# Kernel tuning notes

Hardware: AMD Instinct MI355X
Metric: run time of the kernel (lower is better)

## Reference

```python
import jax, jax.numpy as jnp
import numpy as np

B, C, H, W, D = 2, 96, 64, 64, 32
NUM_HEADS = 8

def setup_inputs() -> dict:
    key = jax.random.key(0)
    kx, kq, kk, kv, kp = jax.random.split(key, 5)
    x = jax.random.normal(kx, (B, C, H, W, D), dtype=jnp.float32)
    # torch nn.Linear weights: [out_features, in_features]; 1x1x1 conv proj as [C_out, C_in]
    s = 0.02
    Wq = jax.random.normal(kq, (C, C), dtype=jnp.float32) * s
    Wk = jax.random.normal(kk, (C, C), dtype=jnp.float32) * s
    Wv = jax.random.normal(kv, (C, C), dtype=jnp.float32) * s
    Wproj = jax.random.normal(kp, (C, C), dtype=jnp.float32) * s
    return {"x": x, "Wq": Wq, "Wk": Wk, "Wv": Wv, "Wproj": Wproj}

def reference(x, Wq, Wk, Wv, Wproj):
    b, c, h, w, d = x.shape
    n = h * w * d
    nh = NUM_HEADS
    hd = c // nh  # head dim (qk_dim == v_dim == dim here)
    # [B, C, H, W, D] -> [B, N, C]
    xf = jnp.transpose(x.reshape(b, c, n), (0, 2, 1))
    def to_heads(W):
        y = jnp.einsum('bnc,oc->bno', xf, W)  # nn.Linear: x @ W^T
        return jnp.transpose(y.reshape(b, n, nh, hd), (0, 2, 1, 3))  # [B, H, N, hd]
    q = to_heads(Wq)
    k = to_heads(Wk)
    v = to_heads(Wv)
    q = jax.nn.softmax(q, axis=-1)   # over head dim
    k = jax.nn.softmax(k, axis=-2)   # over tokens N
    # linear attention: contract over N first -> tiny [B, H, hd, hd] context
    context = jnp.einsum('bhnd,bhne->bhde', k, v)
    attn = jnp.einsum('bhnd,bhde->bhne', q, context)  # [B, H, N, hd]
    out = jnp.transpose(attn, (0, 2, 1, 3)).reshape(b, n, c)  # [B, N, C]
    out = jnp.transpose(out, (0, 2, 1)).reshape(b, c, h, w, d)
    # 1x1x1 conv projection (bias=False) == channel mixing
    out = jnp.einsum('oc,bchwd->bohwd', Wproj, out)
    return out
```

## Files before the change

### kernel.cpp

```cpp
#include <hip/hip_runtime.h>


typedef _Float16 half_t;
typedef _Float16 half8 __attribute__((ext_vector_type(8)));
typedef float f32x4 __attribute__((ext_vector_type(4)));

#define MFMA16 __builtin_amdgcn_mfma_f32_16x16x32_f16
#define NSH 17
#define NP 16

__global__ __launch_bounds__(256, 2)
void p1(const float* __restrict__ x, const float* __restrict__ Wk,
        const float* __restrict__ Wv, float* __restrict__ part) {
  __shared__ __align__(16) char smem[73792];
  half_t* xs  = (half_t*)smem;
  half_t* wsm = (half_t*)(smem + 26624);
  half_t* vl  = (half_t*)smem;
  half_t* ke  = (half_t*)(smem + 46592);

  const int tid  = threadIdx.x;
  const int lane = tid & 63, l15 = lane & 15, quad = lane >> 4, wid = tid >> 6;
  const int b  = blockIdx.x >> 10;
  const int n0 = (blockIdx.x & 1023) << 7;

  {
    const int n = tid & 127, cg = tid >> 7;
    const float* xb = x + (((size_t)(b * 96 + cg * 48)) << NSH) + n0 + n;
#pragma unroll
    for (int i = 0; i < 48; ++i)
      xs[n * 104 + cg * 48 + i] = (half_t)xb[(size_t)i << NSH];
  }
#pragma unroll
  for (int i = 0; i < 36; ++i) {
    int id = i * 256 + tid; int o = id / 96, c = id - o * 96;
    wsm[o * 104 + c] = (half_t)Wk[id];
  }
  __syncthreads();

  f32x4 acc[6][2];
#pragma unroll
  for (int rt = 0; rt < 6; ++rt)
#pragma unroll
    for (int ct = 0; ct < 2; ++ct) acc[rt][ct] = (f32x4){0.f, 0.f, 0.f, 0.f};
#pragma unroll
  for (int ks = 0; ks < 3; ++ks) {
    half8 af[6], bf[2];
#pragma unroll
    for (int rt = 0; rt < 6; ++rt)
      af[rt] = *(const half8*)&wsm[(rt * 16 + l15) * 104 + ks * 32 + quad * 8];
#pragma unroll
    for (int ct = 0; ct < 2; ++ct)
      bf[ct] = *(const half8*)&xs[((wid * 2 + ct) * 16 + l15) * 104 + ks * 32 + quad * 8];
#pragma unroll
    for (int rt = 0; rt < 6; ++rt)
#pragma unroll
      for (int ct = 0; ct < 2; ++ct)
        acc[rt][ct] = MFMA16(af[rt], bf[ct], acc[rt][ct], 0, 0, 0);
  }
#pragma unroll
  for (int rt = 0; rt < 6; ++rt)
#pragma unroll
    for (int ct = 0; ct < 2; ++ct)
#pragma unroll
      for (int i = 0; i < 4; ++i) {
        int row = rt * 16 + quad * 4 + i;
        int col = (wid * 2 + ct) * 16 + l15;
        ke[row * 136 + col] = (half_t)__expf(acc[rt][ct][i]);
      }
  __syncthreads();

#pragma unroll
  for (int i = 0; i < 36; ++i) {
    int id = i * 256 + tid; int o = id / 96, c = id - o * 96;
    wsm[o * 104 + c] = (half_t)Wv[id];
  }
  __syncthreads();

#pragma unroll
  for (int rt = 0; rt < 6; ++rt)
#pragma unroll
    for (int ct = 0; ct < 2; ++ct) acc[rt][ct] = (f32x4){0.f, 0.f, 0.f, 0.f};
#pragma unroll
  for (int ks = 0; ks < 3; ++ks) {
    half8 af[6], bf[2];
#pragma unroll
    for (int rt = 0; rt < 6; ++rt)
      af[rt] = *(const half8*)&wsm[(rt * 16 + l15) * 104 + ks * 32 + quad * 8];
#pragma unroll
    for (int ct = 0; ct < 2; ++ct)
      bf[ct] = *(const half8*)&xs[((wid * 2 + ct) * 16 + l15) * 104 + ks * 32 + quad * 8];
#pragma unroll
    for (int rt = 0; rt < 6; ++rt)
#pragma unroll
      for (int ct = 0; ct < 2; ++ct)
        acc[rt][ct] = MFMA16(af[rt], bf[ct], acc[rt][ct], 0, 0, 0);
  }
  __syncthreads();
#pragma unroll
  for (int rt = 0; rt < 6; ++rt)
#pragma unroll
    for (int ct = 0; ct < 2; ++ct)
#pragma unroll
      for (int i = 0; i < 4; ++i) {
        int row = rt * 16 + quad * 4 + i;
        int col = (wid * 2 + ct) * 16 + l15;
        vl[row * 136 + col] = (half_t)acc[rt][ct][i];
      }
  __syncthreads();

  float* dst = part + (size_t)((blockIdx.x & (NP - 1)) * 2 + b) * 1248;
#pragma unroll
  for (int hh = 0; hh < 2; ++hh) {
    const int h = wid * 2 + hh;
    f32x4 c = (f32x4){0.f, 0.f, 0.f, 0.f};
#pragma unroll
    for (int ks = 0; ks < 4; ++ks) {
      half8 a  = *(const half8*)&ke[(h * 12 + l15) * 136 + ks * 32 + quad * 8];
      half8 bv = *(const half8*)&vl[(h * 12 + l15) * 136 + ks * 32 + quad * 8];
      c = MFMA16(a, bv, c, 0, 0, 0);
    }
#pragma unroll
    for (int i = 0; i < 4; ++i) {
      int d = quad * 4 + i, e = l15;
      if (d < 12 && e < 12) atomicAdd(&dst[h * 144 + d * 12 + e], c[i]);
    }
  }
  if (tid < 96) {
    float s = 0.f;
#pragma unroll
    for (int j = 0; j < 16; ++j) {
      half8 v = *(const half8*)&ke[tid * 136 + j * 8];
#pragma unroll
      for (int e = 0; e < 8; ++e) s += (float)v[e];
    }
    atomicAdd(&dst[1152 + tid], s);
  }
}

__global__ void kB(const float* __restrict__ part, const float* __restrict__ Wproj,
                   float* __restrict__ Mt) {
  const int g = blockIdx.x * 256 + threadIdx.x;
  const int b = g / (96 * 96);
  const int rem = g % (96 * 96);
  const int o = rem / 96;
  const int r = rem % 96;
  const int h = r / 12, d = r % 12;
  float s = 0.f;
#pragma unroll
  for (int p = 0; p < NP; ++p) s += part[(size_t)(p * 2 + b) * 1248 + 1152 + r];
  float acc = 0.f;
#pragma unroll
  for (int e = 0; e < 12; ++e) {
    float ce = 0.f;
#pragma unroll
    for (int p = 0; p < NP; ++p)
      ce += part[(size_t)(p * 2 + b) * 1248 + h * 144 + d * 12 + e];
    acc = fmaf(ce, Wproj[o * 96 + h * 12 + e], acc);
  }
  Mt[(size_t)(b * 96 + o) * 96 + r] = acc / s;
}

__global__ __launch_bounds__(256, 2)
void p3(const float* __restrict__ x, const float* __restrict__ Wq,
        const float* __restrict__ Mt, float* __restrict__ out) {
  __shared__ __align__(16) char smem[66560];
  half_t* xs  = (half_t*)smem;
  half_t* wsm = (half_t*)(smem + 26624);
  half_t* Ms  = (half_t*)(smem + 46592);
  half_t* qs  = (half_t*)smem;

  const int tid  = threadIdx.x;
  const int lane = tid & 63, l15 = lane & 15, quad = lane >> 4, wid = tid >> 6;
  const int b  = blockIdx.x >> 10;
  const int n0 = (blockIdx.x & 1023) << 7;

  {
    const int n = tid & 127, cg = tid >> 7;
    const float* xb = x + (((size_t)(b * 96 + cg * 48)) << NSH) + n0 + n;
#pragma unroll
    for (int i = 0; i < 48; ++i)
      xs[n * 104 + cg * 48 + i] = (half_t)xb[(size_t)i << NSH];
  }
#pragma unroll
  for (int i = 0; i < 36; ++i) {
    int id = i * 256 + tid; int o = id / 96, c = id - o * 96;
    wsm[o * 104 + c] = (half_t)Wq[id];
  }
  {
    const float* mtb = Mt + (size_t)b * 9216;
#pragma unroll
    for (int i = 0; i < 36; ++i) {
      int id = i * 256 + tid; int o = id / 96, r = id - o * 96;
      Ms[o * 104 + r] = (half_t)mtb[id];
    }
  }
  __syncthreads();

  f32x4 acc[6][2];
#pragma unroll
  for (int rt = 0; rt < 6; ++rt)
#pragma unroll
    for (int ct = 0; ct < 2; ++ct) acc[rt][ct] = (f32x4){0.f, 0.f, 0.f, 0.f};
#pragma unroll
  for (int ks = 0; ks < 3; ++ks) {
    half8 af[6], bf[2];
#pragma unroll
    for (int rt = 0; rt < 6; ++rt)
      af[rt] = *(const half8*)&wsm[(rt * 16 + l15) * 104 + ks * 32 + quad * 8];
#pragma unroll
    for (int ct = 0; ct < 2; ++ct)
      bf[ct] = *(const half8*)&xs[((wid * 2 + ct) * 16 + l15) * 104 + ks * 32 + quad * 8];
#pragma unroll
    for (int rt = 0; rt < 6; ++rt)
#pragma unroll
      for (int ct = 0; ct < 2; ++ct)
        acc[rt][ct] = MFMA16(af[rt], bf[ct], acc[rt][ct], 0, 0, 0);
  }
  __syncthreads();
#pragma unroll
  for (int rt = 0; rt < 6; ++rt)
#pragma unroll
    for (int ct = 0; ct < 2; ++ct)
#pragma unroll
      for (int i = 0; i < 4; ++i) {
        int row = rt * 16 + quad * 4 + i;
        int col = (wid * 2 + ct) * 16 + l15;
        qs[col * 104 + row] = (half_t)acc[rt][ct][i];
      }
  __syncthreads();

  {
    const int n = tid & 127, hg = tid >> 7;
    half8 v[6];
#pragma unroll
    for (int j = 0; j < 6; ++j)
      v[j] = *(const half8*)&qs[n * 104 + hg * 48 + j * 8];
    float q[48];
#pragma unroll
    for (int j = 0; j < 6; ++j)
#pragma unroll
      for (int e = 0; e < 8; ++e) q[j * 8 + e] = (float)v[j][e];
#pragma unroll
    for (int hh = 0; hh < 4; ++hh) {
      float* ql = q + hh * 12;
      float m = ql[0];
#pragma unroll
      for (int j = 1; j < 12; ++j) m = fmaxf(m, ql[j]);
      float s = 0.f;
#pragma unroll
      for (int j = 0; j < 12; ++j) { ql[j] = __expf(ql[j] - m); s += ql[j]; }
      const float inv = 1.0f / s;
#pragma unroll
      for (int j = 0; j < 12; ++j) ql[j] *= inv;
    }
#pragma unroll
    for (int j = 0; j < 6; ++j) {
      half8 w;
#pragma unroll
      for (int e = 0; e < 8; ++e) w[e] = (half_t)q[j * 8 + e];
      *(half8*)&qs[n * 104 + hg * 48 + j * 8] = w;
    }
  }
  __syncthreads();

#pragma unroll
  for (int rt = 0; rt < 6; ++rt)
#pragma unroll
    for (int ct = 0; ct < 2; ++ct) acc[rt][ct] = (f32x4){0.f, 0.f, 0.f, 0.f};
#pragma unroll
  for (int ks = 0; ks < 3; ++ks) {
    half8 af[6], bf[2];
#pragma unroll
    for (int rt = 0; rt < 6; ++rt)
      af[rt] = *(const half8*)&Ms[(rt * 16 + l15) * 104 + ks * 32 + quad * 8];
#pragma unroll
    for (int ct = 0; ct < 2; ++ct)
      bf[ct] = *(const half8*)&qs[((wid * 2 + ct) * 16 + l15) * 104 + ks * 32 + quad * 8];
#pragma unroll
    for (int rt = 0; rt < 6; ++rt)
#pragma unroll
      for (int ct = 0; ct < 2; ++ct)
        acc[rt][ct] = MFMA16(af[rt], bf[ct], acc[rt][ct], 0, 0, 0);
  }
#pragma unroll
  for (int rt = 0; rt < 6; ++rt)
#pragma unroll
    for (int ct = 0; ct < 2; ++ct)
#pragma unroll
      for (int i = 0; i < 4; ++i) {
        int row = rt * 16 + quad * 4 + i;
        int col = (wid * 2 + ct) * 16 + l15;
        out[(((size_t)(b * 96 + row)) << NSH) + n0 + col] = acc[rt][ct][i];
      }
}

extern "C" void kernel_launch(void* const* d_in, const int* in_sizes, int n_in,
                              void* d_out, int out_size, void* d_ws, size_t ws_size,
                              hipStream_t stream) {
  const float* x     = (const float*)d_in[0];
  const float* Wq    = (const float*)d_in[1];
  const float* Wk    = (const float*)d_in[2];
  const float* Wv    = (const float*)d_in[3];
  const float* Wproj = (const float*)d_in[4];
  float* out = (float*)d_out;
  float* ws  = (float*)d_ws;

  float* part = ws;
  float* Mt   = ws + NP * 2 * 1248;

  hipMemsetAsync(part, 0, NP * 2 * 1248 * sizeof(float), stream);
  p1<<<2048, 256, 0, stream>>>(x, Wk, Wv, part);
  kB<<<72, 256, 0, stream>>>(part, Wproj, Mt);
  p3<<<2048, 256, 0, stream>>>(x, Wq, Mt, out);
}
```

Baseline: 264.7 us.

## Make p1/p3 persistent over four token tiles with register-resident weights and prefetch

Each block now handles 512 tokens in four 128-token tiles instead of one, so the grid shrinks from 2048 to 512 blocks. Weight fragments (Wk/Wv, Wq, Mt) are converted once into MFMA operand registers rather than staged through shared memory per block. The next tile of x is prefetched into registers while the current tile's MFMAs run, and the context and key-sum partials are accumulated across tiles, which cuts the number of global atomics. p3 now writes its output as vectorized f32x4 stores, and the MFMA operand roles are swapped to match. The trade-off is higher register pressure and fewer blocks to hide latency.

```diff
diff --git a/kernel.cpp b/kernel.cpp
--- a/kernel.cpp
+++ b/kernel.cpp
@@ -2,8 +2,9 @@
 
 
 typedef _Float16 half_t;
-typedef _Float16 half8 __attribute__((ext_vector_type(8)));
-typedef float f32x4 __attribute__((ext_vector_type(4)));
+typedef _Float16 half4v __attribute__((ext_vector_type(4)));
+typedef _Float16 half8  __attribute__((ext_vector_type(8)));
+typedef float    f32x4  __attribute__((ext_vector_type(4)));
 
 #define MFMA16 __builtin_amdgcn_mfma_f32_16x16x32_f16
 #define NSH 17
@@ -12,129 +13,150 @@
 __global__ __launch_bounds__(256, 2)
 void p1(const float* __restrict__ x, const float* __restrict__ Wk,
         const float* __restrict__ Wv, float* __restrict__ part) {
-  __shared__ __align__(16) char smem[73792];
-  half_t* xs  = (half_t*)smem;
-  half_t* wsm = (half_t*)(smem + 26624);
-  half_t* vl  = (half_t*)smem;
-  half_t* ke  = (half_t*)(smem + 46592);
+  __shared__ __align__(16) char smem[79392];
+  half_t* xs = (half_t*)smem;
+  half_t* ke = (half_t*)(smem + 26624);
+  half_t* vl = (half_t*)(smem + 53008);
 
   const int tid  = threadIdx.x;
   const int lane = tid & 63, l15 = lane & 15, quad = lane >> 4, wid = tid >> 6;
-  const int b  = blockIdx.x >> 10;
-  const int n0 = (blockIdx.x & 1023) << 7;
-
+  const int w0 = wid & 1, w1 = wid >> 1;
+  const int b  = blockIdx.x >> 8;
+  const int n0 = (blockIdx.x & 255) << 9;
+  const float* xb = x + (((size_t)b * 96) << NSH);
+
+  half8 wkB[3][3], wvB[3][3];
+#pragma unroll
+  for (int ct = 0; ct < 3; ++ct)
+#pragma unroll
+    for (int ks = 0; ks < 3; ++ks) {
+      const int row = 48 * w1 + ct * 16 + l15;
+      const float* pk = Wk + row * 96 + ks * 32 + quad * 8;
+      const float* pv = Wv + row * 96 + ks * 32 + quad * 8;
+      half8 hk, hv;
+#pragma unroll
+      for (int j = 0; j < 8; ++j) { hk[j] = (half_t)pk[j]; hv[j] = (half_t)pv[j]; }
+      wkB[ct][ks] = hk; wvB[ct][ks] = hv;
+    }
+
+  const int sn = tid & 127, scg = tid >> 7;
   {
-    const int n = tid & 127, cg = tid >> 7;
-    const float* xb = x + (((size_t)(b * 96 + cg * 48)) << NSH) + n0 + n;
+    float xr[48];
 #pragma unroll
     for (int i = 0; i < 48; ++i)
-      xs[n * 104 + cg * 48 + i] = (half_t)xb[(size_t)i << NSH];
-  }
-#pragma unroll
-  for (int i = 0; i < 36; ++i) {
-    int id = i * 256 + tid; int o = id / 96, c = id - o * 96;
-    wsm[o * 104 + c] = (half_t)Wk[id];
-  }
+      xr[i] = xb[(((size_t)(scg * 48 + i)) << NSH) + n0 + sn];
+#pragma unroll
+    for (int j = 0; j < 12; ++j) {
+      half4v h;
+#pragma unroll
+      for (int e = 0; e < 4; ++e) h[e] = (half_t)xr[4 * j + e];
+      *(half4v*)&xs[sn * 104 + scg * 48 + 4 * j] = h;
+    }
+  }
+  f32x4 ctxa[2] = {{0.f,0.f,0.f,0.f},{0.f,0.f,0.f,0.f}};
+  float sacc = 0.f;
   __syncthreads();
 
-  f32x4 acc[6][2];
-#pragma unroll
-  for (int rt = 0; rt < 6; ++rt)
-#pragma unroll
-    for (int ct = 0; ct < 2; ++ct) acc[rt][ct] = (f32x4){0.f, 0.f, 0.f, 0.f};
-#pragma unroll
-  for (int ks = 0; ks < 3; ++ks) {
-    half8 af[6], bf[2];
-#pragma unroll
-    for (int rt = 0; rt < 6; ++rt)
-      af[rt] = *(const half8*)&wsm[(rt * 16 + l15) * 104 + ks * 32 + quad * 8];
-#pragma unroll
-    for (int ct = 0; ct < 2; ++ct)
-      bf[ct] = *(const half8*)&xs[((wid * 2 + ct) * 16 + l15) * 104 + ks * 32 + quad * 8];
-#pragma unroll
-    for (int rt = 0; rt < 6; ++rt)
-#pragma unroll
-      for (int ct = 0; ct < 2; ++ct)
-        acc[rt][ct] = MFMA16(af[rt], bf[ct], acc[rt][ct], 0, 0, 0);
-  }
-#pragma unroll
-  for (int rt = 0; rt < 6; ++rt)
-#pragma unroll
-    for (int ct = 0; ct < 2; ++ct)
-#pragma unroll
-      for (int i = 0; i < 4; ++i) {
-        int row = rt * 16 + quad * 4 + i;
-        int col = (wid * 2 + ct) * 16 + l15;
-        ke[row * 136 + col] = (half_t)__expf(acc[rt][ct][i]);
-      }
-  __syncthreads();
-
-#pragma unroll
-  for (int i = 0; i < 36; ++i) {
-    int id = i * 256 + tid; int o = id / 96, c = id - o * 96;
-    wsm[o * 104 + c] = (half_t)Wv[id];
-  }
-  __syncthreads();
-
-#pragma unroll
-  for (int rt = 0; rt < 6; ++rt)
-#pragma unroll
-    for (int ct = 0; ct < 2; ++ct) acc[rt][ct] = (f32x4){0.f, 0.f, 0.f, 0.f};
-#pragma unroll
-  for (int ks = 0; ks < 3; ++ks) {
-    half8 af[6], bf[2];
-#pragma unroll
-    for (int rt = 0; rt < 6; ++rt)
-      af[rt] = *(const half8*)&wsm[(rt * 16 + l15) * 104 + ks * 32 + quad * 8];
-#pragma unroll
-    for (int ct = 0; ct < 2; ++ct)
-      bf[ct] = *(const half8*)&xs[((wid * 2 + ct) * 16 + l15) * 104 + ks * 32 + quad * 8];
-#pragma unroll
-    for (int rt = 0; rt < 6; ++rt)
-#pragma unroll
-      for (int ct = 0; ct < 2; ++ct)
-        acc[rt][ct] = MFMA16(af[rt], bf[ct], acc[rt][ct], 0, 0, 0);
-  }
-  __syncthreads();
-#pragma unroll
-  for (int rt = 0; rt < 6; ++rt)
-#pragma unroll
-    for (int ct = 0; ct < 2; ++ct)
-#pragma unroll
-      for (int i = 0; i < 4; ++i) {
-        int row = rt * 16 + quad * 4 + i;
-        int col = (wid * 2 + ct) * 16 + l15;
-        vl[row * 136 + col] = (half_t)acc[rt][ct][i];
-      }
-  __syncthreads();
-
+  for (int t = 0; t < 4; ++t) {
+    float xr[48];
+    if (t < 3) {
+#pragma unroll
+      for (int i = 0; i < 48; ++i)
+        xr[i] = xb[(((size_t)(scg * 48 + i)) << NSH) + n0 + (t + 1) * 128 + sn];
+    }
+    f32x4 acc[4][3];
+#pragma unroll
+    for (int rt = 0; rt < 4; ++rt)
+#pragma unroll
+      for (int ct = 0; ct < 3; ++ct) acc[rt][ct] = (f32x4){0.f,0.f,0.f,0.f};
+#pragma unroll
+    for (int ks = 0; ks < 3; ++ks) {
+      half8 af[4];
+#pragma unroll
+      for (int rt = 0; rt < 4; ++rt)
+        af[rt] = *(const half8*)&xs[(64 * w0 + rt * 16 + l15) * 104 + ks * 32 + quad * 8];
+#pragma unroll
+      for (int rt = 0; rt < 4; ++rt)
+#pragma unroll
+        for (int ct = 0; ct < 3; ++ct)
+          acc[rt][ct] = MFMA16(af[rt], wkB[ct][ks], acc[rt][ct], 0, 0, 0);
+    }
+#pragma unroll
+    for (int rt = 0; rt < 4; ++rt)
+#pragma unroll
+      for (int ct = 0; ct < 3; ++ct) {
+        half4v h;
+#pragma unroll
+        for (int i = 0; i < 4; ++i) h[i] = (half_t)__expf(acc[rt][ct][i]);
+        *(half4v*)&ke[(48 * w1 + ct * 16 + l15) * 136 + 64 * w0 + rt * 16 + quad * 4] = h;
+      }
+#pragma unroll
+    for (int rt = 0; rt < 4; ++rt)
+#pragma unroll
+      for (int ct = 0; ct < 3; ++ct) acc[rt][ct] = (f32x4){0.f,0.f,0.f,0.f};
+#pragma unroll
+    for (int ks = 0; ks < 3; ++ks) {
+      half8 af[4];
+#pragma unroll
+      for (int rt = 0; rt < 4; ++rt)
+        af[rt] = *(const half8*)&xs[(64 * w0 + rt * 16 + l15) * 104 + ks * 32 + quad * 8];
+#pragma unroll
+      for (int rt = 0; rt < 4; ++rt)
+#pragma unroll
+        for (int ct = 0; ct < 3; ++ct)
+          acc[rt][ct] = MFMA16(af[rt], wvB[ct][ks], acc[rt][ct], 0, 0, 0);
+    }
+#pragma unroll
+    for (int rt = 0; rt < 4; ++rt)
+#pragma unroll
+      for (int ct = 0; ct < 3; ++ct) {
+        half4v h;
+#pragma unroll
+        for (int i = 0; i < 4; ++i) h[i] = (half_t)acc[rt][ct][i];
+        *(half4v*)&vl[(48 * w1 + ct * 16 + l15) * 136 + 64 * w0 + rt * 16 + quad * 4] = h;
+      }
+    __syncthreads();
+    if (t < 3) {
+#pragma unroll
+      for (int j = 0; j < 12; ++j) {
+        half4v h;
+#pragma unroll
+        for (int e = 0; e < 4; ++e) h[e] = (half_t)xr[4 * j + e];
+        *(half4v*)&xs[sn * 104 + scg * 48 + 4 * j] = h;
+      }
+    }
+#pragma unroll
+    for (int hh = 0; hh < 2; ++hh) {
+      int rr = (wid * 2 + hh) * 12 + l15; rr = rr > 96 ? 96 : rr;
+#pragma unroll
+      for (int ks = 0; ks < 4; ++ks) {
+        half8 a  = *(const half8*)&ke[rr * 136 + ks * 32 + quad * 8];
+        half8 bv = *(const half8*)&vl[rr * 136 + ks * 32 + quad * 8];
+        ctxa[hh] = MFMA16(a, bv, ctxa[hh], 0, 0, 0);
+      }
+    }
+    if (tid < 192) {
+      const int c = tid >> 1, seg = tid & 1;
+#pragma unroll
+      for (int j = 0; j < 8; ++j) {
+        half8 v = *(const half8*)&ke[c * 136 + seg * 64 + j * 8];
+#pragma unroll
+        for (int e = 0; e < 8; ++e) sacc += (float)v[e];
+      }
+    }
+    __syncthreads();
+  }
   float* dst = part + (size_t)((blockIdx.x & (NP - 1)) * 2 + b) * 1248;
 #pragma unroll
   for (int hh = 0; hh < 2; ++hh) {
-    const int h = wid * 2 + hh;
-    f32x4 c = (f32x4){0.f, 0.f, 0.f, 0.f};
-#pragma unroll
-    for (int ks = 0; ks < 4; ++ks) {
-      half8 a  = *(const half8*)&ke[(h * 12 + l15) * 136 + ks * 32 + quad * 8];
-      half8 bv = *(const half8*)&vl[(h * 12 + l15) * 136 + ks * 32 + quad * 8];
-      c = MFMA16(a, bv, c, 0, 0, 0);
-    }
 #pragma unroll
     for (int i = 0; i < 4; ++i) {
-      int d = quad * 4 + i, e = l15;
-      if (d < 12 && e < 12) atomicAdd(&dst[h * 144 + d * 12 + e], c[i]);
-    }
-  }
-  if (tid < 96) {
-    float s = 0.f;
-#pragma unroll
-    for (int j = 0; j < 16; ++j) {
-      half8 v = *(const half8*)&ke[tid * 136 + j * 8];
-#pragma unroll
-      for (int e = 0; e < 8; ++e) s += (float)v[e];
-    }
-    atomicAdd(&dst[1152 + tid], s);
-  }
+      const int d = quad * 4 + i, e = l15;
+      if (d < 12 && e < 12)
+        atomicAdd(&dst[(wid * 2 + hh) * 144 + d * 12 + e], ctxa[hh][i]);
+    }
+  }
+  if (tid < 192) atomicAdd(&dst[1152 + (tid >> 1)], sacc);
 }
 
 __global__ void kB(const float* __restrict__ part, const float* __restrict__ Wproj,
@@ -163,135 +185,161 @@
 __global__ __launch_bounds__(256, 2)
 void p3(const float* __restrict__ x, const float* __restrict__ Wq,
         const float* __restrict__ Mt, float* __restrict__ out) {
-  __shared__ __align__(16) char smem[66560];
-  half_t* xs  = (half_t*)smem;
-  half_t* wsm = (half_t*)(smem + 26624);
-  half_t* Ms  = (half_t*)(smem + 46592);
-  half_t* qs  = (half_t*)smem;
+  __shared__ __align__(16) char smem[53248];
+  half_t* xs = (half_t*)smem;
+  half_t* qs = (half_t*)(smem + 26624);
 
   const int tid  = threadIdx.x;
   const int lane = tid & 63, l15 = lane & 15, quad = lane >> 4, wid = tid >> 6;
-  const int b  = blockIdx.x >> 10;
-  const int n0 = (blockIdx.x & 1023) << 7;
-
-  {
-    const int n = tid & 127, cg = tid >> 7;
-    const float* xb = x + (((size_t)(b * 96 + cg * 48)) << NSH) + n0 + n;
-#pragma unroll
-    for (int i = 0; i < 48; ++i)
-      xs[n * 104 + cg * 48 + i] = (half_t)xb[(size_t)i << NSH];
-  }
-#pragma unroll
-  for (int i = 0; i < 36; ++i) {
-    int id = i * 256 + tid; int o = id / 96, c = id - o * 96;
-    wsm[o * 104 + c] = (half_t)Wq[id];
-  }
+  const int w0 = wid & 1, w1 = wid >> 1;
+  const int b  = blockIdx.x >> 8;
+  const int n0 = (blockIdx.x & 255) << 9;
+  const float* xb = x + (((size_t)b * 96) << NSH);
+
+  half8 aw[3][3];
+#pragma unroll
+  for (int rt = 0; rt < 3; ++rt)
+#pragma unroll
+    for (int ks = 0; ks < 3; ++ks) {
+      const float* pq = Wq + (48 * w0 + rt * 16 + l15) * 96 + ks * 32 + quad * 8;
+      half8 h;
+#pragma unroll
+      for (int j = 0; j < 8; ++j) h[j] = (half_t)pq[j];
+      aw[rt][ks] = h;
+    }
+  half8 mB[3][3];
   {
     const float* mtb = Mt + (size_t)b * 9216;
 #pragma unroll
-    for (int i = 0; i < 36; ++i) {
-      int id = i * 256 + tid; int o = id / 96, r = id - o * 96;
-      Ms[o * 104 + r] = (half_t)mtb[id];
+    for (int ct = 0; ct < 3; ++ct)
+#pragma unroll
+      for (int ks = 0; ks < 3; ++ks) {
+        const float* pm = mtb + (48 * w1 + ct * 16 + l15) * 96 + ks * 32 + quad * 8;
+        half8 h;
+#pragma unroll
+        for (int j = 0; j < 8; ++j) h[j] = (half_t)pm[j];
+        mB[ct][ks] = h;
+      }
+  }
+
+  const int sn = tid & 127, scg = tid >> 7;
+  {
+    float xr[48];
+#pragma unroll
+    for (int i = 0; i < 48; ++i)
+      xr[i] = xb[(((size_t)(scg * 48 + i)) << NSH) + n0 + sn];
+#pragma unroll
+    for (int j = 0; j < 12; ++j) {
+      half4v h;
+#pragma unroll
+      for (int e = 0; e < 4; ++e) h[e] = (half_t)xr[4 * j + e];
+      *(half4v*)&xs[sn * 104 + scg * 48 + 4 * j] = h;
     }
   }
   __syncthreads();
 
-  f32x4 acc[6][2];
-#pragma unroll
-  for (int rt = 0; rt < 6; ++rt)
-#pragma unroll
-    for (int ct = 0; ct < 2; ++ct) acc[rt][ct] = (f32x4){0.f, 0.f, 0.f, 0.f};
-#pragma unroll
-  for (int ks = 0; ks < 3; ++ks) {
-    half8 af[6], bf[2];
-#pragma unroll
-    for (int rt = 0; rt < 6; ++rt)
-      af[rt] = *(const half8*)&wsm[(rt * 16 + l15) * 104 + ks * 32 + quad * 8];
-#pragma unroll
-    for (int ct = 0; ct < 2; ++ct)
-      bf[ct] = *(const half8*)&xs[((wid * 2 + ct) * 16 + l15) * 104 + ks * 32 + quad * 8];
-#pragma unroll
-    for (int rt = 0; rt < 6; ++rt)
-#pragma unroll
-      for (int ct = 0; ct < 2; ++ct)
-        acc[rt][ct] = MFMA16(af[rt], bf[ct], acc[rt][ct], 0, 0, 0);
-  }
-  __syncthreads();
-#pragma unroll
-  for (int rt = 0; rt < 6; ++rt)
-#pragma unroll
-    for (int ct = 0; ct < 2; ++ct)
-#pragma unroll
-      for (int i = 0; i < 4; ++i) {
-        int row = rt * 16 + quad * 4 + i;
-        int col = (wid * 2 + ct) * 16 + l15;
-        qs[col * 104 + row] = (half_t)acc[rt][ct][i];
-      }
-  __syncthreads();
-
-  {
-    const int n = tid & 127, hg = tid >> 7;
-    half8 v[6];
-#pragma unroll
-    for (int j = 0; j < 6; ++j)
-      v[j] = *(const half8*)&qs[n * 104 + hg * 48 + j * 8];
-    float q[48];
-#pragma unroll
-    for (int j = 0; j < 6; ++j)
-#pragma unroll
-      for (int e = 0; e < 8; ++e) q[j * 8 + e] = (float)v[j][e];
-#pragma unroll
-    for (int hh = 0; hh < 4; ++hh) {
-      float* ql = q + hh * 12;
-      float m = ql[0];
-#pragma unroll
-      for (int j = 1; j < 12; ++j) m = fmaxf(m, ql[j]);
-      float s = 0.f;
-#pragma unroll
-      for (int j = 0; j < 12; ++j) { ql[j] = __expf(ql[j] - m); s += ql[j]; }
-      const float inv = 1.0f / s;
-#pragma unroll
-      for (int j = 0; j < 12; ++j) ql[j] *= inv;
-    }
-#pragma unroll
-    for (int j = 0; j < 6; ++j) {
-      half8 w;
-#pragma unroll
-      for (int e = 0; e < 8; ++e) w[e] = (half_t)q[j * 8 + e];
-      *(half8*)&qs[n * 104 + hg * 48 + j * 8] = w;
-    }
-  }
-  __syncthreads();
-
-#pragma unroll
-  for (int rt = 0; rt < 6; ++rt)
-#pragma unroll
-    for (int ct = 0; ct < 2; ++ct) acc[rt][ct] = (f32x4){0.f, 0.f, 0.f, 0.f};
-#pragma unroll
-  for (int ks = 0; ks < 3; ++ks) {
-    half8 af[6], bf[2];
-#pragma unroll
-    for (int rt = 0; rt < 6; ++rt)
-      af[rt] = *(const half8*)&Ms[(rt * 16 + l15) * 104 + ks * 32 + quad * 8];
-#pragma unroll
-    for (int ct = 0; ct < 2; ++ct)
-      bf[ct] = *(const half8*)&qs[((wid * 2 + ct) * 16 + l15) * 104 + ks * 32 + quad * 8];
-#pragma unroll
-    for (int rt = 0; rt < 6; ++rt)
-#pragma unroll
-      for (int ct = 0; ct < 2; ++ct)
-        acc[rt][ct] = MFMA16(af[rt], bf[ct], acc[rt][ct], 0, 0, 0);
-  }
-#pragma unroll
-  for (int rt = 0; rt < 6; ++rt)
-#pragma unroll
-    for (int ct = 0; ct < 2; ++ct)
-#pragma unroll
-      for (int i = 0; i < 4; ++i) {
-        int row = rt * 16 + quad * 4 + i;
-        int col = (wid * 2 + ct) * 16 + l15;
-        out[(((size_t)(b * 96 + row)) << NSH) + n0 + col] = acc[rt][ct][i];
-      }
+  for (int t = 0; t < 4; ++t) {
+    float xr[48];
+    if (t < 3) {
+#pragma unroll
+      for (int i = 0; i < 48; ++i)
+        xr[i] = xb[(((size_t)(scg * 48 + i)) << NSH) + n0 + (t + 1) * 128 + sn];
+    }
+    f32x4 qacc[3][4];
+#pragma unroll
+    for (int rt = 0; rt < 3; ++rt)
+#pragma unroll
+      for (int ct = 0; ct < 4; ++ct) qacc[rt][ct] = (f32x4){0.f,0.f,0.f,0.f};
+#pragma unroll
+    for (int ks = 0; ks < 3; ++ks) {
+      half8 bf[4];
+#pragma unroll
+      for (int ct = 0; ct < 4; ++ct)
+        bf[ct] = *(const half8*)&xs[(64 * w1 + ct * 16 + l15) * 104 + ks * 32 + quad * 8];
+#pragma unroll
+      for (int rt = 0; rt < 3; ++rt)
+#pragma unroll
+        for (int ct = 0; ct < 4; ++ct)
+          qacc[rt][ct] = MFMA16(aw[rt][ks], bf[ct], qacc[rt][ct], 0, 0, 0);
+    }
+#pragma unroll
+    for (int rt = 0; rt < 3; ++rt)
+#pragma unroll
+      for (int ct = 0; ct < 4; ++ct) {
+        half4v h;
+#pragma unroll
+        for (int i = 0; i < 4; ++i) h[i] = (half_t)qacc[rt][ct][i];
+        *(half4v*)&qs[(64 * w1 + ct * 16 + l15) * 104 + 48 * w0 + rt * 16 + quad * 4] = h;
+      }
+    __syncthreads();
+    {
+      const int n = tid & 127, g = tid >> 7;
+      float q[48];
+#pragma unroll
+      for (int j = 0; j < 12; ++j) {
+        half4v v = *(const half4v*)&qs[n * 104 + g * 48 + j * 4];
+#pragma unroll
+        for (int e = 0; e < 4; ++e) q[j * 4 + e] = (float)v[e];
+      }
+#pragma unroll
+      for (int hh = 0; hh < 4; ++hh) {
+        float* ql = q + hh * 12;
+        float m = ql[0];
+#pragma unroll
+        for (int j = 1; j < 12; ++j) m = fmaxf(m, ql[j]);
+        float s = 0.f;
+#pragma unroll
+        for (int j = 0; j < 12; ++j) { ql[j] = __expf(ql[j] - m); s += ql[j]; }
+        const float inv = 1.0f / s;
+#pragma unroll
+        for (int j = 0; j < 12; ++j) ql[j] *= inv;
+      }
+#pragma unroll
+      for (int j = 0; j < 12; ++j) {
+        half4v v;
+#pragma unroll
+        for (int e = 0; e < 4; ++e) v[e] = (half_t)q[j * 4 + e];
+        *(half4v*)&qs[n * 104 + g * 48 + j * 4] = v;
+      }
+    }
+    if (t < 3) {
+#pragma unroll
+      for (int j = 0; j < 12; ++j) {
+        half4v h;
+#pragma unroll
+        for (int e = 0; e < 4; ++e) h[e] = (half_t)xr[4 * j + e];
+        *(half4v*)&xs[sn * 104 + scg * 48 + 4 * j] = h;
+      }
+    }
+    __syncthreads();
+    f32x4 oacc[4][3];
+#pragma unroll
+    for (int rt = 0; rt < 4; ++rt)
+#pragma unroll
+      for (int ct = 0; ct < 3; ++ct) oacc[rt][ct] = (f32x4){0.f,0.f,0.f,0.f};
+#pragma unroll
+    for (int ks = 0; ks < 3; ++ks) {
+      half8 af[4];
+#pragma unroll
+      for (int rt = 0; rt < 4; ++rt)
+        af[rt] = *(const half8*)&qs[(64 * w0 + rt * 16 + l15) * 104 + ks * 32 + quad * 8];
+#pragma unroll
+      for (int rt = 0; rt < 4; ++rt)
+#pragma unroll
+        for (int ct = 0; ct < 3; ++ct)
+          oacc[rt][ct] = MFMA16(af[rt], mB[ct][ks], oacc[rt][ct], 0, 0, 0);
+    }
+#pragma unroll
+    for (int rt = 0; rt < 4; ++rt)
+#pragma unroll
+      for (int ct = 0; ct < 3; ++ct) {
+        const int o  = 48 * w1 + ct * 16 + l15;
+        const size_t off = (((size_t)(b * 96 + o)) << NSH)
+                         + n0 + t * 128 + 64 * w0 + rt * 16 + quad * 4;
+        *(f32x4*)&out[off] = oacc[rt][ct];
+      }
+    __syncthreads();
+  }
 }
 
 extern "C" void kernel_launch(void* const* d_in, const int* in_sizes, int n_in,
@@ -309,7 +357,7 @@
   float* Mt   = ws + NP * 2 * 1248;
 
   hipMemsetAsync(part, 0, NP * 2 * 1248 * sizeof(float), stream);
-  p1<<<2048, 256, 0, stream>>>(x, Wk, Wv, part);
+  p1<<<512, 256, 0, stream>>>(x, Wk, Wv, part);
   kB<<<72, 256, 0, stream>>>(part, Wproj, Mt);
-  p3<<<2048, 256, 0, stream>>>(x, Wq, Mt, out);
+  p3<<<512, 256, 0, stream>>>(x, Wq, Mt, out);
 }
```

Result: slower. 272.7 us (+3.0%).
